# Kernel optimization log

Measured on AMD Instinct MI355X. Metric: run time of the kernel, lower is better.

Reference implementation:

```python
import jax, jax.numpy as jnp
import numpy as np

N = 2_097_152          # sampled points
H = 16                 # hash heads / levels
F = 2                  # features per head
M = 524_288            # 2**19 table size
HID = 64               # mlp width
OUT = 3


def setup_inputs() -> dict:
    key = jax.random.key(0)
    ks = jax.random.split(key, 12)
    idx = jax.random.randint(ks[0], (N, H), 0, M, dtype=jnp.int64)
    tables = jax.random.normal(ks[1], (H, M, F), dtype=jnp.float32) * 0.02
    d_in = H * F  # 32
    def lin(k, d1, d2):
        kw, kb = jax.random.split(k)
        s = 1.0 / np.sqrt(d1)
        W = jax.random.uniform(kw, (d1, d2), jnp.float32, -s, s)
        b = jax.random.uniform(kb, (d2,), jnp.float32, -s, s)
        return W, b
    W1, b1 = lin(ks[2], d_in, HID)
    W2, b2 = lin(ks[3], HID, HID)
    W3, b3 = lin(ks[4], HID, HID)
    W4, b4 = lin(ks[5], HID, OUT)
    return {"idx": idx, "tables": tables,
            "W1": W1, "b1": b1, "W2": W2, "b2": b2,
            "W3": W3, "b3": b3, "W4": W4, "b4": b4}


def reference(idx, tables, W1, b1, W2, b2, W3, b3, W4, b4):
    # per-head gather: tables[h][idx[:, h]] -> [N, H, F], then concat heads
    gather = jax.vmap(lambda t, i: t[i], in_axes=(0, 1), out_axes=1)
    x = gather(tables, idx).reshape(idx.shape[0], -1)  # [N, H*F]
    x = jax.nn.relu(x @ W1 + b1)
    x = jax.nn.relu(x @ W2 + b2)
    x = jax.nn.relu(x @ W3 + b3)
    return x @ W4 + b4  # [N, 3]
```

## Files before the change

kernel.cpp:

```cpp
#include <hip/hip_runtime.h>
#include <hip/hip_bf16.h>

typedef __attribute__((ext_vector_type(8))) short short8;
typedef __attribute__((ext_vector_type(4))) float floatx4;
typedef __attribute__((ext_vector_type(4))) int int4v;
typedef __attribute__((ext_vector_type(4))) unsigned int uint4v;

#define MTBL 524288
#define HSTRIDE 72

union U4S8 { uint4v u; short8 s; };

static __device__ __forceinline__ unsigned int pack2bf(float a, float b) {
    union { float f; unsigned int u; } x, y;
    x.f = a; y.f = b;
    unsigned int lo = (x.u + 0x8000u) >> 16;
    unsigned int hi = (y.u + 0x8000u) & 0xFFFF0000u;
    return lo | hi;
}
static __device__ __forceinline__ short bf1(float a) {
    union { float f; unsigned int u; } x;
    x.f = a;
    return (short)((x.u + 0x8000u) >> 16);
}

__global__ __launch_bounds__(256) void ngp_compress(
    const floatx4* __restrict__ tab4, unsigned int* __restrict__ tblC)
{
    const int t = blockIdx.x * 256 + threadIdx.x;
    floatx4 a = __builtin_nontemporal_load(tab4 + (size_t)2 * t);
    floatx4 b = __builtin_nontemporal_load(tab4 + (size_t)2 * t + 1);
    uint4v w;
    w[0] = pack2bf(a[0], a[1]);
    w[1] = pack2bf(a[2], a[3]);
    w[2] = pack2bf(b[0], b[1]);
    w[3] = pack2bf(b[2], b[3]);
    __builtin_nontemporal_store(w, (uint4v*)(tblC + (size_t)4 * t));
}

__global__ __launch_bounds__(256) void ngp_transpose(
    const int* __restrict__ idx, int* __restrict__ idxT, int N)
{
    const int t  = blockIdx.x * 256 + threadIdx.x;
    const int p0 = t * 4;
    const int4v* rows = (const int4v*)idx;
    int4v r[4][4];
#pragma unroll
    for (int p = 0; p < 4; ++p)
#pragma unroll
        for (int c = 0; c < 4; ++c)
            r[p][c] = __builtin_nontemporal_load(rows + (size_t)(p0 + p) * 4 + c);
#pragma unroll
    for (int c = 0; c < 4; ++c)
#pragma unroll
        for (int k = 0; k < 4; ++k) {
            const int h = c * 4 + k;
            int4v w;
            w[0] = r[0][c][k]; w[1] = r[1][c][k]; w[2] = r[2][c][k]; w[3] = r[3][c][k];
            __builtin_nontemporal_store(w, (int4v*)(idxT + (size_t)h * N + p0));
        }
}

__global__ __launch_bounds__(256) void ngp_gather_ph(
    const int* __restrict__ idxT, const unsigned int* __restrict__ tblC,
    unsigned int* __restrict__ xU, int N, int phase, int iters)
{
    const int h    = ((blockIdx.x & 7) << 1) | phase;
    const int slot = blockIdx.x >> 3;
    const int* __restrict__ ih = idxT + (size_t)h * N;
    const unsigned int* __restrict__ th = tblC + (size_t)h * MTBL;
    unsigned int* __restrict__ xh = xU + (size_t)h * N;

    int p = slot * (N >> 8) + (threadIdx.x << 3);
    int4v iv0 = __builtin_nontemporal_load((const int4v*)(ih + p));
    int4v iv1 = __builtin_nontemporal_load((const int4v*)(ih + p + 4));
    for (int it = 0; it < iters; ++it) {
        int4v nv0, nv1;
        if (it + 1 < iters) {
            nv0 = __builtin_nontemporal_load((const int4v*)(ih + p + 2048));
            nv1 = __builtin_nontemporal_load((const int4v*)(ih + p + 2052));
        }
        uint4v w0, w1;
        w0[0] = th[iv0[0]]; w0[1] = th[iv0[1]]; w0[2] = th[iv0[2]]; w0[3] = th[iv0[3]];
        w1[0] = th[iv1[0]]; w1[1] = th[iv1[1]]; w1[2] = th[iv1[2]]; w1[3] = th[iv1[3]];
        __builtin_nontemporal_store(w0, (uint4v*)(xh + p));
        __builtin_nontemporal_store(w1, (uint4v*)(xh + p + 4));
        iv0 = nv0; iv1 = nv1;
        p += 2048;
    }
}

__global__ __launch_bounds__(256, 2) void ngp_mlp(
    const unsigned int* __restrict__ xU,
    const float* __restrict__ W1, const float* __restrict__ b1,
    const float* __restrict__ W2, const float* __restrict__ b2,
    const float* __restrict__ W3, const float* __restrict__ b3,
    const float* __restrict__ W4, const float* __restrict__ b4,
    float* __restrict__ out, int N, int tiles_per_wave)
{
    __shared__ float sW[6144];
    __shared__ __hip_bfloat16 sH[4][16 * HSTRIDE];

    const int tid  = threadIdx.x;
    const int wave = tid >> 6;
    const int lane = tid & 63;
    const int q = lane >> 4;
    const int m = lane & 15;

    short8 A1[4], A2[4][2], A3[4][2], A4[2];
    floatx4 C1[4], C2[4], C3[4], C4;

    for (int i = tid; i < 2048; i += 256) sW[i] = W1[i];
    for (int i = tid; i < 4096; i += 256) sW[2048 + i] = W2[i];
    __syncthreads();
#pragma unroll
    for (int t = 0; t < 4; ++t) {
        short8 a;
#pragma unroll
        for (int j = 0; j < 8; ++j)
            a[j] = bf1(sW[(q * 8 + j) * 64 + t * 16 + m]);
        A1[t] = a;
    }
#pragma unroll
    for (int t = 0; t < 4; ++t)
#pragma unroll
        for (int c = 0; c < 2; ++c) {
            short8 a;
#pragma unroll
            for (int j = 0; j < 8; ++j)
                a[j] = bf1(sW[2048 + (c * 32 + q * 8 + j) * 64 + t * 16 + m]);
            A2[t][c] = a;
        }
    __syncthreads();

    for (int i = tid; i < 4096; i += 256) sW[i] = W3[i];
    if (tid < 192) sW[4096 + tid] = W4[tid];
    if (tid < 64)       sW[4288 + tid] = b1[tid];
    else if (tid < 128) sW[4288 + tid] = b2[tid - 64];
    else if (tid < 192) sW[4288 + tid] = b3[tid - 128];
    else if (tid < 195) sW[4288 + tid] = b4[tid - 192];
    __syncthreads();
#pragma unroll
    for (int t = 0; t < 4; ++t)
#pragma unroll
        for (int c = 0; c < 2; ++c) {
            short8 a;
#pragma unroll
            for (int j = 0; j < 8; ++j)
                a[j] = bf1(sW[(c * 32 + q * 8 + j) * 64 + t * 16 + m]);
            A3[t][c] = a;
        }
#pragma unroll
    for (int c = 0; c < 2; ++c) {
        short8 a;
#pragma unroll
        for (int j = 0; j < 8; ++j)
            a[j] = (m < 3) ? bf1(sW[4096 + (c * 32 + q * 8 + j) * 3 + m]) : (short)0;
        A4[c] = a;
    }
#pragma unroll
    for (int t = 0; t < 4; ++t)
#pragma unroll
        for (int r = 0; r < 4; ++r) {
            C1[t][r] = sW[4288 + t * 16 + q * 4 + r];
            C2[t][r] = sW[4288 + 64 + t * 16 + q * 4 + r];
            C3[t][r] = sW[4288 + 128 + t * 16 + q * 4 + r];
        }
#pragma unroll
    for (int r = 0; r < 4; ++r)
        C4[r] = (q == 0 && r < 3) ? sW[4288 + 192 + r] : 0.0f;

    __hip_bfloat16* hrow = &sH[wave][m * HSTRIDE];
    const int gw = blockIdx.x * 4 + wave;
    const int tile0 = gw * tiles_per_wave;

    const unsigned int* xr = xU + (size_t)(q * 4) * N + m;

    uint4v cur;
    {
        const int c0 = tile0 * 16;
        cur[0] = xr[c0];
        cur[1] = xr[(size_t)N + c0];
        cur[2] = xr[(size_t)2 * N + c0];
        cur[3] = xr[(size_t)3 * N + c0];
    }

    for (int it = 0; it < tiles_per_wave; ++it) {
        const int pbase = (tile0 + it) * 16;
        const bool more = (it + 1) < tiles_per_wave;

        U4S8 bx; bx.u = cur;
        const short8 Bx = bx.s;

        uint4v nxt;
        if (more) {
            const int cn = pbase + 16;
            nxt[0] = xr[cn];
            nxt[1] = xr[(size_t)N + cn];
            nxt[2] = xr[(size_t)2 * N + cn];
            nxt[3] = xr[(size_t)3 * N + cn];
        }

        floatx4 acc[4];
#pragma unroll
        for (int t = 0; t < 4; ++t)
            acc[t] = __builtin_amdgcn_mfma_f32_16x16x32_bf16(A1[t], Bx, C1[t], 0, 0, 0);

#pragma unroll
        for (int t = 0; t < 4; ++t) {
            uint2 pk;
            pk.x = pack2bf(fmaxf(acc[t][0], 0.f), fmaxf(acc[t][1], 0.f));
            pk.y = pack2bf(fmaxf(acc[t][2], 0.f), fmaxf(acc[t][3], 0.f));
            *(uint2*)(hrow + t * 16 + q * 4) = pk;
        }
        short8 Bh0 = *(const short8*)(hrow + q * 8);
        short8 Bh1 = *(const short8*)(hrow + 32 + q * 8);

#pragma unroll
        for (int t = 0; t < 4; ++t) {
            acc[t] = __builtin_amdgcn_mfma_f32_16x16x32_bf16(A2[t][0], Bh0, C2[t], 0, 0, 0);
            acc[t] = __builtin_amdgcn_mfma_f32_16x16x32_bf16(A2[t][1], Bh1, acc[t], 0, 0, 0);
        }

#pragma unroll
        for (int t = 0; t < 4; ++t) {
            uint2 pk;
            pk.x = pack2bf(fmaxf(acc[t][0], 0.f), fmaxf(acc[t][1], 0.f));
            pk.y = pack2bf(fmaxf(acc[t][2], 0.f), fmaxf(acc[t][3], 0.f));
            *(uint2*)(hrow + t * 16 + q * 4) = pk;
        }
        Bh0 = *(const short8*)(hrow + q * 8);
        Bh1 = *(const short8*)(hrow + 32 + q * 8);

#pragma unroll
        for (int t = 0; t < 4; ++t) {
            acc[t] = __builtin_amdgcn_mfma_f32_16x16x32_bf16(A3[t][0], Bh0, C3[t], 0, 0, 0);
            acc[t] = __builtin_amdgcn_mfma_f32_16x16x32_bf16(A3[t][1], Bh1, acc[t], 0, 0, 0);
        }

#pragma unroll
        for (int t = 0; t < 4; ++t) {
            uint2 pk;
            pk.x = pack2bf(fmaxf(acc[t][0], 0.f), fmaxf(acc[t][1], 0.f));
            pk.y = pack2bf(fmaxf(acc[t][2], 0.f), fmaxf(acc[t][3], 0.f));
            *(uint2*)(hrow + t * 16 + q * 4) = pk;
        }
        Bh0 = *(const short8*)(hrow + q * 8);
        Bh1 = *(const short8*)(hrow + 32 + q * 8);

        floatx4 o;
        o = __builtin_amdgcn_mfma_f32_16x16x32_bf16(A4[0], Bh0, C4, 0, 0, 0);
        o = __builtin_amdgcn_mfma_f32_16x16x32_bf16(A4[1], Bh1, o, 0, 0, 0);

        if (q == 0) {
            const int pn = pbase + m;
            out[pn * 3 + 0] = o[0];
            out[pn * 3 + 1] = o[1];
            out[pn * 3 + 2] = o[2];
        }

        cur = nxt;
    }
}

__global__ __launch_bounds__(256, 2) void ngp_fused(
    const int* __restrict__ idx,
    const float* __restrict__ tables,
    const float* __restrict__ W1, const float* __restrict__ b1,
    const float* __restrict__ W2, const float* __restrict__ b2,
    const float* __restrict__ W3, const float* __restrict__ b3,
    const float* __restrict__ W4, const float* __restrict__ b4,
    float* __restrict__ out, int tiles_per_wave)
{
    __shared__ float sW1[2048];
    __shared__ float sW2[4096];
    __shared__ float sW3[4096];
    __shared__ float sW4[192];
    __shared__ float sB[200];
    __shared__ __hip_bfloat16 sH[4][16 * HSTRIDE];

    const int tid = threadIdx.x;
    for (int i = tid; i < 2048; i += 256) sW1[i] = W1[i];
    for (int i = tid; i < 4096; i += 256) sW2[i] = W2[i];
    for (int i = tid; i < 4096; i += 256) sW3[i] = W3[i];
    if (tid < 192) sW4[tid] = W4[tid];
    if (tid < 64)       sB[tid] = b1[tid];
    else if (tid < 128) sB[tid] = b2[tid - 64];
    else if (tid < 192) sB[tid] = b3[tid - 128];
    else if (tid < 195) sB[tid] = b4[tid - 192];
    __syncthreads();

    const int wave = tid >> 6;
    const int lane = tid & 63;
    const int q = lane >> 4;
    const int m = lane & 15;

    short8 A1[4], A2[4][2], A3[4][2], A4[2];
#pragma unroll
    for (int t = 0; t < 4; ++t) {
        short8 a;
#pragma unroll
        for (int j = 0; j < 8; ++j)
            a[j] = bf1(sW1[(q * 8 + j) * 64 + t * 16 + m]);
        A1[t] = a;
    }
#pragma unroll
    for (int t = 0; t < 4; ++t)
#pragma unroll
        for (int c = 0; c < 2; ++c) {
            short8 a, a3;
#pragma unroll
            for (int j = 0; j < 8; ++j) {
                a[j]  = bf1(sW2[(c * 32 + q * 8 + j) * 64 + t * 16 + m]);
                a3[j] = bf1(sW3[(c * 32 + q * 8 + j) * 64 + t * 16 + m]);
            }
            A2[t][c] = a;
            A3[t][c] = a3;
        }
#pragma unroll
    for (int c = 0; c < 2; ++c) {
        short8 a;
#pragma unroll
        for (int j = 0; j < 8; ++j)
            a[j] = (m < 3) ? bf1(sW4[(c * 32 + q * 8 + j) * 3 + m]) : (short)0;
        A4[c] = a;
    }

    floatx4 C1[4], C2[4], C3[4], C4;
#pragma unroll
    for (int t = 0; t < 4; ++t)
#pragma unroll
        for (int r = 0; r < 4; ++r) {
            C1[t][r] = sB[t * 16 + q * 4 + r];
            C2[t][r] = sB[64 + t * 16 + q * 4 + r];
            C3[t][r] = sB[128 + t * 16 + q * 4 + r];
        }
#pragma unroll
    for (int r = 0; r < 4; ++r)
        C4[r] = (q == 0 && r < 3) ? sB[192 + r] : 0.0f;

    __hip_bfloat16* hrow = &sH[wave][m * HSTRIDE];
    const int4*   idx4 = (const int4*)idx;
    const float2* tbl  = (const float2*)tables;

    const int gw = blockIdx.x * 4 + wave;
    const int tile0 = gw * tiles_per_wave;

    int4 iv = idx4[(tile0 * 16 + m) * 4 + q];
    float2 g0 = tbl[(q * 4 + 0) * MTBL + iv.x];
    float2 g1 = tbl[(q * 4 + 1) * MTBL + iv.y];
    float2 g2 = tbl[(q * 4 + 2) * MTBL + iv.z];
    float2 g3 = tbl[(q * 4 + 3) * MTBL + iv.w];

    for (int it = 0; it < tiles_per_wave; ++it) {
        const int pbase = (tile0 + it) * 16;
        const bool more = (it + 1) < tiles_per_wave;

        short8 Bx;
        {
            unsigned int p0 = pack2bf(g0.x, g0.y);
            unsigned int p1 = pack2bf(g1.x, g1.y);
            unsigned int p2 = pack2bf(g2.x, g2.y);
            unsigned int p3 = pack2bf(g3.x, g3.y);
            Bx[0] = (short)(p0 & 0xFFFF); Bx[1] = (short)(p0 >> 16);
            Bx[2] = (short)(p1 & 0xFFFF); Bx[3] = (short)(p1 >> 16);
            Bx[4] = (short)(p2 & 0xFFFF); Bx[5] = (short)(p2 >> 16);
            Bx[6] = (short)(p3 & 0xFFFF); Bx[7] = (short)(p3 >> 16);
        }

        int4 ivn;
        if (more) ivn = idx4[((pbase + 16) + m) * 4 + q];

        floatx4 acc[4];
#pragma unroll
        for (int t = 0; t < 4; ++t)
            acc[t] = __builtin_amdgcn_mfma_f32_16x16x32_bf16(A1[t], Bx, C1[t], 0, 0, 0);

#pragma unroll
        for (int t = 0; t < 4; ++t) {
            uint2 pk;
            pk.x = pack2bf(fmaxf(acc[t][0], 0.f), fmaxf(acc[t][1], 0.f));
            pk.y = pack2bf(fmaxf(acc[t][2], 0.f), fmaxf(acc[t][3], 0.f));
            *(uint2*)(hrow + t * 16 + q * 4) = pk;
        }
        short8 Bh0 = *(const short8*)(hrow + q * 8);
        short8 Bh1 = *(const short8*)(hrow + 32 + q * 8);

#pragma unroll
        for (int t = 0; t < 4; ++t) {
            acc[t] = __builtin_amdgcn_mfma_f32_16x16x32_bf16(A2[t][0], Bh0, C2[t], 0, 0, 0);
            acc[t] = __builtin_amdgcn_mfma_f32_16x16x32_bf16(A2[t][1], Bh1, acc[t], 0, 0, 0);
        }

        if (more) {
            g0 = tbl[(q * 4 + 0) * MTBL + ivn.x];
            g1 = tbl[(q * 4 + 1) * MTBL + ivn.y];
            g2 = tbl[(q * 4 + 2) * MTBL + ivn.z];
            g3 = tbl[(q * 4 + 3) * MTBL + ivn.w];
        }

#pragma unroll
        for (int t = 0; t < 4; ++t) {
            uint2 pk;
            pk.x = pack2bf(fmaxf(acc[t][0], 0.f), fmaxf(acc[t][1], 0.f));
            pk.y = pack2bf(fmaxf(acc[t][2], 0.f), fmaxf(acc[t][3], 0.f));
            *(uint2*)(hrow + t * 16 + q * 4) = pk;
        }
        Bh0 = *(const short8*)(hrow + q * 8);
        Bh1 = *(const short8*)(hrow + 32 + q * 8);

#pragma unroll
        for (int t = 0; t < 4; ++t) {
            acc[t] = __builtin_amdgcn_mfma_f32_16x16x32_bf16(A3[t][0], Bh0, C3[t], 0, 0, 0);
            acc[t] = __builtin_amdgcn_mfma_f32_16x16x32_bf16(A3[t][1], Bh1, acc[t], 0, 0, 0);
        }

#pragma unroll
        for (int t = 0; t < 4; ++t) {
            uint2 pk;
            pk.x = pack2bf(fmaxf(acc[t][0], 0.f), fmaxf(acc[t][1], 0.f));
            pk.y = pack2bf(fmaxf(acc[t][2], 0.f), fmaxf(acc[t][3], 0.f));
            *(uint2*)(hrow + t * 16 + q * 4) = pk;
        }
        Bh0 = *(const short8*)(hrow + q * 8);
        Bh1 = *(const short8*)(hrow + 32 + q * 8);

        floatx4 o;
        o = __builtin_amdgcn_mfma_f32_16x16x32_bf16(A4[0], Bh0, C4, 0, 0, 0);
        o = __builtin_amdgcn_mfma_f32_16x16x32_bf16(A4[1], Bh1, o, 0, 0, 0);

        if (q == 0) {
            const int pn = pbase + m;
            out[pn * 3 + 0] = o[0];
            out[pn * 3 + 1] = o[1];
            out[pn * 3 + 2] = o[2];
        }
    }
}

extern "C" void kernel_launch(void* const* d_in, const int* in_sizes, int n_in,
                              void* d_out, int out_size, void* d_ws, size_t ws_size,
                              hipStream_t stream) {
    const int*   idx    = (const int*)d_in[0];
    const float* tables = (const float*)d_in[1];
    const float* W1 = (const float*)d_in[2];
    const float* b1 = (const float*)d_in[3];
    const float* W2 = (const float*)d_in[4];
    const float* b2 = (const float*)d_in[5];
    const float* W3 = (const float*)d_in[6];
    const float* b3 = (const float*)d_in[7];
    const float* W4 = (const float*)d_in[8];
    const float* b4 = (const float*)d_in[9];
    float* out = (float*)d_out;

    const int N = in_sizes[0] / 16;
    const int total_tiles = N / 16;

    const size_t idxT_bytes = (size_t)16 * N * 4;
    const size_t xU_bytes   = (size_t)16 * N * 4;
    const size_t tblC_bytes = (size_t)16 * MTBL * 4;
    const size_t need = idxT_bytes + xU_bytes + tblC_bytes;

    if (ws_size >= need) {
        int*          idxT = (int*)d_ws;
        unsigned int* xU   = (unsigned int*)((char*)d_ws + idxT_bytes);
        unsigned int* tblC = (unsigned int*)((char*)d_ws + idxT_bytes + xU_bytes);

        ngp_transpose<<<N / 1024, 256, 0, stream>>>(idx, idxT, N);
        ngp_compress<<<(16 * MTBL) / 1024, 256, 0, stream>>>(
            (const floatx4*)tables, tblC);
        const int iters = (N >> 8) >> 11;
        ngp_gather_ph<<<2048, 256, 0, stream>>>(idxT, tblC, xU, N, 0, iters);
        ngp_gather_ph<<<2048, 256, 0, stream>>>(idxT, tblC, xU, N, 1, iters);
        const int blocks = 2048;
        const int tiles_per_wave = total_tiles / (blocks * 4);
        ngp_mlp<<<blocks, 256, 0, stream>>>(xU, W1, b1, W2, b2, W3, b3, W4, b4,
                                            out, N, tiles_per_wave);
    } else {
        const int blocks = 2048;
        const int tiles_per_wave = total_tiles / (blocks * 4);
        ngp_fused<<<blocks, 256, 0, stream>>>(idx, tables, W1, b1, W2, b2, W3, b3,
                                              W4, b4, out, tiles_per_wave);
    }
}
```

Before: 649.9 us.

## Merge prep kernels, widen gather per thread, interleave two MLP tiles per wave

```diff
diff --git a/kernel.cpp b/kernel.cpp
--- a/kernel.cpp
+++ b/kernel.cpp
@@ -12,53 +12,60 @@
 union U4S8 { uint4v u; short8 s; };
 
 static __device__ __forceinline__ unsigned int pack2bf(float a, float b) {
-    union { float f; unsigned int u; } x, y;
-    x.f = a; y.f = b;
-    unsigned int lo = (x.u + 0x8000u) >> 16;
-    unsigned int hi = (y.u + 0x8000u) & 0xFFFF0000u;
-    return lo | hi;
+    unsigned int ua = __float_as_uint(a) + 0x8000u;
+    unsigned int ub = __float_as_uint(b) + 0x8000u;
+    return __builtin_amdgcn_perm(ub, ua, 0x07060302u);
 }
 static __device__ __forceinline__ short bf1(float a) {
-    union { float f; unsigned int u; } x;
-    x.f = a;
-    return (short)((x.u + 0x8000u) >> 16);
-}
-
-__global__ __launch_bounds__(256) void ngp_compress(
-    const floatx4* __restrict__ tab4, unsigned int* __restrict__ tblC)
+    return (short)((__float_as_uint(a) + 0x8000u) >> 16);
+}
+
+static __device__ __forceinline__ void store_h(__hip_bfloat16* hrow,
+                                               const floatx4* acc, int q) {
+#pragma unroll
+    for (int t = 0; t < 4; ++t) {
+        uint2 pk;
+        pk.x = pack2bf(fmaxf(acc[t][0], 0.f), fmaxf(acc[t][1], 0.f));
+        pk.y = pack2bf(fmaxf(acc[t][2], 0.f), fmaxf(acc[t][3], 0.f));
+        *(uint2*)(hrow + t * 16 + q * 4) = pk;
+    }
+}
+
+__global__ __launch_bounds__(256) void ngp_prep(
+    const int* __restrict__ idx, int* __restrict__ idxT,
+    const floatx4* __restrict__ tab4, unsigned int* __restrict__ tblC, int N)
 {
-    const int t = blockIdx.x * 256 + threadIdx.x;
-    floatx4 a = __builtin_nontemporal_load(tab4 + (size_t)2 * t);
-    floatx4 b = __builtin_nontemporal_load(tab4 + (size_t)2 * t + 1);
-    uint4v w;
-    w[0] = pack2bf(a[0], a[1]);
-    w[1] = pack2bf(a[2], a[3]);
-    w[2] = pack2bf(b[0], b[1]);
-    w[3] = pack2bf(b[2], b[3]);
-    __builtin_nontemporal_store(w, (uint4v*)(tblC + (size_t)4 * t));
-}
-
-__global__ __launch_bounds__(256) void ngp_transpose(
-    const int* __restrict__ idx, int* __restrict__ idxT, int N)
-{
-    const int t  = blockIdx.x * 256 + threadIdx.x;
-    const int p0 = t * 4;
-    const int4v* rows = (const int4v*)idx;
-    int4v r[4][4];
-#pragma unroll
-    for (int p = 0; p < 4; ++p)
+    const int TB = N >> 10;
+    if ((int)blockIdx.x < TB) {
+        const int t  = blockIdx.x * 256 + threadIdx.x;
+        const int p0 = t * 4;
+        const int4v* rows = (const int4v*)idx;
+        int4v r[4][4];
+#pragma unroll
+        for (int p = 0; p < 4; ++p)
+#pragma unroll
+            for (int c = 0; c < 4; ++c)
+                r[p][c] = __builtin_nontemporal_load(rows + (size_t)(p0 + p) * 4 + c);
 #pragma unroll
         for (int c = 0; c < 4; ++c)
-            r[p][c] = __builtin_nontemporal_load(rows + (size_t)(p0 + p) * 4 + c);
-#pragma unroll
-    for (int c = 0; c < 4; ++c)
-#pragma unroll
-        for (int k = 0; k < 4; ++k) {
-            const int h = c * 4 + k;
-            int4v w;
-            w[0] = r[0][c][k]; w[1] = r[1][c][k]; w[2] = r[2][c][k]; w[3] = r[3][c][k];
-            __builtin_nontemporal_store(w, (int4v*)(idxT + (size_t)h * N + p0));
-        }
+#pragma unroll
+            for (int k = 0; k < 4; ++k) {
+                const int h = c * 4 + k;
+                int4v w;
+                w[0] = r[0][c][k]; w[1] = r[1][c][k]; w[2] = r[2][c][k]; w[3] = r[3][c][k];
+                *(int4v*)(idxT + (size_t)h * N + p0) = w;
+            }
+    } else {
+        const int t = (blockIdx.x - TB) * 256 + threadIdx.x;
+        floatx4 a = __builtin_nontemporal_load(tab4 + (size_t)2 * t);
+        floatx4 b = __builtin_nontemporal_load(tab4 + (size_t)2 * t + 1);
+        uint4v w;
+        w[0] = pack2bf(a[0], a[1]);
+        w[1] = pack2bf(a[2], a[3]);
+        w[2] = pack2bf(b[0], b[1]);
+        w[3] = pack2bf(b[2], b[3]);
+        *(uint4v*)(tblC + (size_t)4 * t) = w;
+    }
 }
 
 __global__ __launch_bounds__(256) void ngp_gather_ph(
@@ -71,22 +78,28 @@
     const unsigned int* __restrict__ th = tblC + (size_t)h * MTBL;
     unsigned int* __restrict__ xh = xU + (size_t)h * N;
 
-    int p = slot * (N >> 8) + (threadIdx.x << 3);
-    int4v iv0 = __builtin_nontemporal_load((const int4v*)(ih + p));
-    int4v iv1 = __builtin_nontemporal_load((const int4v*)(ih + p + 4));
+    int p = slot * (N >> 8) + (threadIdx.x << 4);
+    int4v iv[4];
+#pragma unroll
+    for (int j = 0; j < 4; ++j)
+        iv[j] = __builtin_nontemporal_load((const int4v*)(ih + p + 4 * j));
     for (int it = 0; it < iters; ++it) {
-        int4v nv0, nv1;
+        int4v nv[4];
         if (it + 1 < iters) {
-            nv0 = __builtin_nontemporal_load((const int4v*)(ih + p + 2048));
-            nv1 = __builtin_nontemporal_load((const int4v*)(ih + p + 2052));
-        }
-        uint4v w0, w1;
-        w0[0] = th[iv0[0]]; w0[1] = th[iv0[1]]; w0[2] = th[iv0[2]]; w0[3] = th[iv0[3]];
-        w1[0] = th[iv1[0]]; w1[1] = th[iv1[1]]; w1[2] = th[iv1[2]]; w1[3] = th[iv1[3]];
-        __builtin_nontemporal_store(w0, (uint4v*)(xh + p));
-        __builtin_nontemporal_store(w1, (uint4v*)(xh + p + 4));
-        iv0 = nv0; iv1 = nv1;
-        p += 2048;
+#pragma unroll
+            for (int j = 0; j < 4; ++j)
+                nv[j] = __builtin_nontemporal_load((const int4v*)(ih + p + 4096 + 4 * j));
+        }
+#pragma unroll
+        for (int j = 0; j < 4; ++j) {
+            uint4v w;
+            w[0] = th[iv[j][0]]; w[1] = th[iv[j][1]];
+            w[2] = th[iv[j][2]]; w[3] = th[iv[j][3]];
+            __builtin_nontemporal_store(w, (uint4v*)(xh + p + 4 * j));
+        }
+#pragma unroll
+        for (int j = 0; j < 4; ++j) iv[j] = nv[j];
+        p += 4096;
     }
 }
 
@@ -98,8 +111,7 @@
     const float* __restrict__ W4, const float* __restrict__ b4,
     float* __restrict__ out, int N, int tiles_per_wave)
 {
-    __shared__ float sW[6144];
-    __shared__ __hip_bfloat16 sH[4][16 * HSTRIDE];
+    __shared__ __align__(16) float sW[6144];
 
     const int tid  = threadIdx.x;
     const int wave = tid >> 6;
@@ -169,97 +181,95 @@
 #pragma unroll
     for (int r = 0; r < 4; ++r)
         C4[r] = (q == 0 && r < 3) ? sW[4288 + 192 + r] : 0.0f;
-
-    __hip_bfloat16* hrow = &sH[wave][m * HSTRIDE];
+    __syncthreads();
+
+    __hip_bfloat16* hA = (__hip_bfloat16*)sW + wave * (32 * HSTRIDE) + m * HSTRIDE;
+    __hip_bfloat16* hB = hA + 16 * HSTRIDE;
+
     const int gw = blockIdx.x * 4 + wave;
     const int tile0 = gw * tiles_per_wave;
-
     const unsigned int* xr = xU + (size_t)(q * 4) * N + m;
 
-    uint4v cur;
+    uint4v curA, curB;
     {
-        const int c0 = tile0 * 16;
-        cur[0] = xr[c0];
-        cur[1] = xr[(size_t)N + c0];
-        cur[2] = xr[(size_t)2 * N + c0];
-        cur[3] = xr[(size_t)3 * N + c0];
-    }
-
-    for (int it = 0; it < tiles_per_wave; ++it) {
-        const int pbase = (tile0 + it) * 16;
-        const bool more = (it + 1) < tiles_per_wave;
-
-        U4S8 bx; bx.u = cur;
-        const short8 Bx = bx.s;
-
-        uint4v nxt;
+        const int cA = tile0 * 16, cB = cA + 16;
+        curA[0] = xr[cA]; curA[1] = xr[(size_t)N + cA];
+        curA[2] = xr[(size_t)2 * N + cA]; curA[3] = xr[(size_t)3 * N + cA];
+        curB[0] = xr[cB]; curB[1] = xr[(size_t)N + cB];
+        curB[2] = xr[(size_t)2 * N + cB]; curB[3] = xr[(size_t)3 * N + cB];
+    }
+
+    for (int it = 0; it < tiles_per_wave; it += 2) {
+        const int pA = (tile0 + it) * 16;
+        const bool more = (it + 2) < tiles_per_wave;
+
+        U4S8 ba; ba.u = curA; const short8 BxA = ba.s;
+        U4S8 bb; bb.u = curB; const short8 BxB = bb.s;
+
+        uint4v nA, nB;
         if (more) {
-            const int cn = pbase + 16;
-            nxt[0] = xr[cn];
-            nxt[1] = xr[(size_t)N + cn];
-            nxt[2] = xr[(size_t)2 * N + cn];
-            nxt[3] = xr[(size_t)3 * N + cn];
-        }
-
-        floatx4 acc[4];
-#pragma unroll
-        for (int t = 0; t < 4; ++t)
-            acc[t] = __builtin_amdgcn_mfma_f32_16x16x32_bf16(A1[t], Bx, C1[t], 0, 0, 0);
-
+            const int cA = pA + 32, cB = pA + 48;
+            nA[0] = xr[cA]; nA[1] = xr[(size_t)N + cA];
+            nA[2] = xr[(size_t)2 * N + cA]; nA[3] = xr[(size_t)3 * N + cA];
+            nB[0] = xr[cB]; nB[1] = xr[(size_t)N + cB];
+            nB[2] = xr[(size_t)2 * N + cB]; nB[3] = xr[(size_t)3 * N + cB];
+        }
+
+        floatx4 aA[4], aB[4];
 #pragma unroll
         for (int t = 0; t < 4; ++t) {
-            uint2 pk;
-            pk.x = pack2bf(fmaxf(acc[t][0], 0.f), fmaxf(acc[t][1], 0.f));
-            pk.y = pack2bf(fmaxf(acc[t][2], 0.f), fmaxf(acc[t][3], 0.f));
-            *(uint2*)(hrow + t * 16 + q * 4) = pk;
-        }
-        short8 Bh0 = *(const short8*)(hrow + q * 8);
-        short8 Bh1 = *(const short8*)(hrow + 32 + q * 8);
+            aA[t] = __builtin_amdgcn_mfma_f32_16x16x32_bf16(A1[t], BxA, C1[t], 0, 0, 0);
+            aB[t] = __builtin_amdgcn_mfma_f32_16x16x32_bf16(A1[t], BxB, C1[t], 0, 0, 0);
+        }
+        store_h(hA, aA, q); store_h(hB, aB, q);
+        short8 fA0 = *(const short8*)(hA + q * 8);
+        short8 fA1 = *(const short8*)(hA + 32 + q * 8);
+        short8 fB0 = *(const short8*)(hB + q * 8);
+        short8 fB1 = *(const short8*)(hB + 32 + q * 8);
 
 #pragma unroll
         for (int t = 0; t < 4; ++t) {
-            acc[t] = __builtin_amdgcn_mfma_f32_16x16x32_bf16(A2[t][0], Bh0, C2[t], 0, 0, 0);
-            acc[t] = __builtin_amdgcn_mfma_f32_16x16x32_bf16(A2[t][1], Bh1, acc[t], 0, 0, 0);
-        }
+            aA[t] = __builtin_amdgcn_mfma_f32_16x16x32_bf16(A2[t][0], fA0, C2[t], 0, 0, 0);
+            aA[t] = __builtin_amdgcn_mfma_f32_16x16x32_bf16(A2[t][1], fA1, aA[t], 0, 0, 0);
+            aB[t] = __builtin_amdgcn_mfma_f32_16x16x32_bf16(A2[t][0], fB0, C2[t], 0, 0, 0);
+            aB[t] = __builtin_amdgcn_mfma_f32_16x16x32_bf16(A2[t][1], fB1, aB[t], 0, 0, 0);
+        }
+        store_h(hA, aA, q); store_h(hB, aB, q);
+        fA0 = *(const short8*)(hA + q * 8);
+        fA1 = *(const short8*)(hA + 32 + q * 8);
+        fB0 = *(const short8*)(hB + q * 8);
+        fB1 = *(const short8*)(hB + 32 + q * 8);
 
 #pragma unroll
         for (int t = 0; t < 4; ++t) {
-            uint2 pk;
-            pk.x = pack2bf(fmaxf(acc[t][0], 0.f), fmaxf(acc[t][1], 0.f));
-            pk.y = pack2bf(fmaxf(acc[t][2], 0.f), fmaxf(acc[t][3], 0.f));
-            *(uint2*)(hrow + t * 16 + q * 4) = pk;
-        }
-        Bh0 = *(const short8*)(hrow + q * 8);
-        Bh1 = *(const short8*)(hrow + 32 + q * 8);
-
-#pragma unroll
-        for (int t = 0; t < 4; ++t) {
-            acc[t] = __builtin_amdgcn_mfma_f32_16x16x32_bf16(A3[t][0], Bh0, C3[t], 0, 0, 0);
-            acc[t] = __builtin_amdgcn_mfma_f32_16x16x32_bf16(A3[t][1], Bh1, acc[t], 0, 0, 0);
-        }
-
-#pragma unroll
-        for (int t = 0; t < 4; ++t) {
-            uint2 pk;
-            pk.x = pack2bf(fmaxf(acc[t][0], 0.f), fmaxf(acc[t][1], 0.f));
-            pk.y = pack2bf(fmaxf(acc[t][2], 0.f), fmaxf(acc[t][3], 0.f));
-            *(uint2*)(hrow + t * 16 + q * 4) = pk;
-        }
-        Bh0 = *(const short8*)(hrow + q * 8);
-        Bh1 = *(const short8*)(hrow + 32 + q * 8);
-
-        floatx4 o;
-        o = __builtin_amdgcn_mfma_f32_16x16x32_bf16(A4[0], Bh0, C4, 0, 0, 0);
-        o = __builtin_amdgcn_mfma_f32_16x16x32_bf16(A4[1], Bh1, o, 0, 0, 0);
+            aA[t] = __builtin_amdgcn_mfma_f32_16x16x32_bf16(A3[t][0], fA0, C3[t], 0, 0, 0);
+            aA[t] = __builtin_amdgcn_mfma_f32_16x16x32_bf16(A3[t][1], fA1, aA[t], 0, 0, 0);
+            aB[t] = __builtin_amdgcn_mfma_f32_16x16x32_bf16(A3[t][0], fB0, C3[t], 0, 0, 0);
+            aB[t] = __builtin_amdgcn_mfma_f32_16x16x32_bf16(A3[t][1], fB1, aB[t], 0, 0, 0);
+        }
+        store_h(hA, aA, q); store_h(hB, aB, q);
+        fA0 = *(const short8*)(hA + q * 8);
+        fA1 = *(const short8*)(hA + 32 + q * 8);
+        fB0 = *(const short8*)(hB + q * 8);
+        fB1 = *(const short8*)(hB + 32 + q * 8);
+
+        floatx4 oA, oB;
+        oA = __builtin_amdgcn_mfma_f32_16x16x32_bf16(A4[0], fA0, C4, 0, 0, 0);
+        oA = __builtin_amdgcn_mfma_f32_16x16x32_bf16(A4[1], fA1, oA, 0, 0, 0);
+        oB = __builtin_amdgcn_mfma_f32_16x16x32_bf16(A4[0], fB0, C4, 0, 0, 0);
+        oB = __builtin_amdgcn_mfma_f32_16x16x32_bf16(A4[1], fB1, oB, 0, 0, 0);
 
         if (q == 0) {
-            const int pn = pbase + m;
-            out[pn * 3 + 0] = o[0];
-            out[pn * 3 + 1] = o[1];
-            out[pn * 3 + 2] = o[2];
-        }
-
-        cur = nxt;
+            const int pnA = pA + m, pnB = pA + 16 + m;
+            out[pnA * 3 + 0] = oA[0];
+            out[pnA * 3 + 1] = oA[1];
+            out[pnA * 3 + 2] = oA[2];
+            out[pnB * 3 + 0] = oB[0];
+            out[pnB * 3 + 1] = oB[1];
+            out[pnB * 3 + 2] = oB[2];
+        }
+
+        curA = nA; curB = nB;
     }
 }
 
@@ -376,13 +386,7 @@
         for (int t = 0; t < 4; ++t)
             acc[t] = __builtin_amdgcn_mfma_f32_16x16x32_bf16(A1[t], Bx, C1[t], 0, 0, 0);
 
-#pragma unroll
-        for (int t = 0; t < 4; ++t) {
-            uint2 pk;
-            pk.x = pack2bf(fmaxf(acc[t][0], 0.f), fmaxf(acc[t][1], 0.f));
-            pk.y = pack2bf(fmaxf(acc[t][2], 0.f), fmaxf(acc[t][3], 0.f));
-            *(uint2*)(hrow + t * 16 + q * 4) = pk;
-        }
+        store_h(hrow, acc, q);
         short8 Bh0 = *(const short8*)(hrow + q * 8);
         short8 Bh1 = *(const short8*)(hrow + 32 + q * 8);
 
@@ -399,13 +403,7 @@
             g3 = tbl[(q * 4 + 3) * MTBL + ivn.w];
         }
 
-#pragma unroll
-        for (int t = 0; t < 4; ++t) {
-            uint2 pk;
-            pk.x = pack2bf(fmaxf(acc[t][0], 0.f), fmaxf(acc[t][1], 0.f));
-            pk.y = pack2bf(fmaxf(acc[t][2], 0.f), fmaxf(acc[t][3], 0.f));
-            *(uint2*)(hrow + t * 16 + q * 4) = pk;
-        }
+        store_h(hrow, acc, q);
         Bh0 = *(const short8*)(hrow + q * 8);
         Bh1 = *(const short8*)(hrow + 32 + q * 8);
 
@@ -415,13 +413,7 @@
             acc[t] = __builtin_amdgcn_mfma_f32_16x16x32_bf16(A3[t][1], Bh1, acc[t], 0, 0, 0);
         }
 
-#pragma unroll
-        for (int t = 0; t < 4; ++t) {
-            uint2 pk;
-            pk.x = pack2bf(fmaxf(acc[t][0], 0.f), fmaxf(acc[t][1], 0.f));
-            pk.y = pack2bf(fmaxf(acc[t][2], 0.f), fmaxf(acc[t][3], 0.f));
-            *(uint2*)(hrow + t * 16 + q * 4) = pk;
-        }
+        store_h(hrow, acc, q);
         Bh0 = *(const short8*)(hrow + q * 8);
         Bh1 = *(const short8*)(hrow + 32 + q * 8);
 
@@ -466,10 +458,11 @@
         unsigned int* xU   = (unsigned int*)((char*)d_ws + idxT_bytes);
         unsigned int* tblC = (unsigned int*)((char*)d_ws + idxT_bytes + xU_bytes);
 
-        ngp_transpose<<<N / 1024, 256, 0, stream>>>(idx, idxT, N);
-        ngp_compress<<<(16 * MTBL) / 1024, 256, 0, stream>>>(
-            (const floatx4*)tables, tblC);
-        const int iters = (N >> 8) >> 11;
+        const int TB = N >> 10;
+        const int CB = (16 * MTBL) >> 10;
+        ngp_prep<<<TB + CB, 256, 0, stream>>>(idx, idxT, (const floatx4*)tables,
+                                              tblC, N);
+        const int iters = (N >> 8) >> 12;
         ngp_gather_ph<<<2048, 256, 0, stream>>>(idxT, tblC, xU, N, 0, iters);
         ngp_gather_ph<<<2048, 256, 0, stream>>>(idxT, tblC, xU, N, 1, iters);
         const int blocks = 2048;
```

New measurement: 679.5 us. 1.05x slower.
